# Kernel tuning notes

Hardware: AMD Instinct MI355X
Metric: run time of the kernel (lower is better)

The kernel has to match this reference:

```python
import jax, jax.numpy as jnp
import numpy as np

EPS = 1e-5

def setup_inputs() -> dict:
    key = jax.random.key(0)
    ks = jax.random.split(key, 8)
    B, T, D, S = 8, 4096, 1024, 64
    return {
        "x": jax.random.normal(ks[0], (B, T, D), dtype=jnp.float32),
        "time_decay": jax.random.normal(ks[1], (S,), dtype=jnp.float32) * 0.1 - 0.5,
        "time_first": jax.random.normal(ks[2], (S,), dtype=jnp.float32) * 0.1,
        "W_key": jax.random.normal(ks[3], (S, D), dtype=jnp.float32) * 0.02,
        "W_value": jax.random.normal(ks[4], (S, D), dtype=jnp.float32) * 0.02,
        "W_output": jax.random.normal(ks[5], (D, S), dtype=jnp.float32) * 0.02,
        "W_shift": jax.random.normal(ks[6], (D, D), dtype=jnp.float32) * 0.02,
        "shift_gate": jnp.ones((D,), dtype=jnp.float32),
        "ln_w": jnp.ones((D,), dtype=jnp.float32),
        "ln_b": jnp.zeros((D,), dtype=jnp.float32),
    }


def _forward(x, time_decay, time_first, W_key, W_value, W_output, W_shift, shift_gate, ln_w, ln_b):
    B, T, D = x.shape
    S = time_decay.shape[0]
    # --- token shift: rotate sequence by shift_len, project, gated blend ---
    shift_len = max(1, int(T * 0.5))
    x_cat = jnp.concatenate([x[:, shift_len:], x[:, :-shift_len]], axis=1)  # (B,T,D)
    gate = jax.nn.sigmoid(shift_gate)
    x_shift = jnp.einsum('btd,ed->bte', x_cat, W_shift) * gate + x * (1.0 - gate)
    # --- layernorm (torch: biased variance, eps=1e-5) ---
    mu = jnp.mean(x_shift, axis=-1, keepdims=True)
    var = jnp.mean(jnp.square(x_shift - mu), axis=-1, keepdims=True)
    xn = (x_shift - mu) * jax.lax.rsqrt(var + EPS) * ln_w + ln_b
    # --- key/value projections and per-step wkv (fully vectorized) ---
    k = jnp.einsum('btd,sd->bts', xn, W_key)    # (B,T,S)
    v = jnp.einsum('btd,sd->bts', xn, W_value)  # (B,T,S)
    wkv = jnp.exp(-jnp.exp(time_first) * jax.nn.sigmoid(k)) * v  # (B,T,S)
    # --- linear recurrence: state = state*w + wkv_t, scanned over T ---
    w = jnp.exp(time_decay)  # (S,)
    def step(state, wkv_t):
        state = state * w + wkv_t
        return state, state
    init = jnp.zeros((B, S), dtype=x.dtype)
    last_state, states = jax.lax.scan(step, init, jnp.swapaxes(wkv, 0, 1))  # states: (T,B,S)
    states = jnp.swapaxes(states, 0, 1)  # (B,T,S)
    # --- batched output projection (applied per-step in torch; same math) ---
    output = jnp.einsum('bts,ds->btd', states, W_output)  # (B,T,D)
    return output, last_state


def reference(x, time_decay, time_first, W_key, W_value, W_output, W_shift, shift_gate, ln_w, ln_b):
    out, last_state = _forward(x, time_decay, time_first, W_key, W_value, W_output, W_shift, shift_gate, ln_w, ln_b)
    return out, jax.lax.stop_gradient(last_state)
```

## Files before the change

### kernel.cpp

```cpp
#include <hip/hip_runtime.h>
#include <stdint.h>

#define B_ 8
#define T_ 4096
#define D_ 1024
#define S_ 64
#define N_ 32768
#define OUT_ELEMS 33554432
#define NCHK 128
#define CHKL 32

typedef __attribute__((ext_vector_type(8))) short bf16x8;
typedef __attribute__((ext_vector_type(8))) unsigned short u16x8;
typedef __attribute__((ext_vector_type(4))) float f32x4;

__device__ __forceinline__ uint16_t f2bf(float f) {
    union { float f; uint32_t u; } v; v.f = f;
    uint32_t r = v.u + 0x7FFFu + ((v.u >> 16) & 1u);
    return (uint16_t)(r >> 16);
}
__device__ __forceinline__ float bf2f(uint16_t h) {
    union { uint32_t u; float f; } v; v.u = ((uint32_t)h) << 16;
    return v.f;
}

#define GLOAD_LDS16(gp, lp)                                             \
    __builtin_amdgcn_global_load_lds(                                   \
        (const __attribute__((address_space(1))) void*)(gp),            \
        (__attribute__((address_space(3))) void*)(lp), 16, 0, 0)

__global__ void prep(const float* __restrict__ x,
                     const float* __restrict__ Wsf, const float* __restrict__ Wkf,
                     const float* __restrict__ Wvf, const float* __restrict__ Wof,
                     const float* __restrict__ sg, const float* __restrict__ tf,
                     const float* __restrict__ lnw, const float* __restrict__ lnb,
                     uint16_t* __restrict__ xb, uint16_t* __restrict__ Wsb,
                     uint16_t* __restrict__ Wkvb, uint16_t* __restrict__ Wob,
                     float* __restrict__ gbuf, float* __restrict__ efirst,
                     float* __restrict__ ucvec)
{
    __shared__ float red[4];
    const int blk = blockIdx.x, tid = threadIdx.x;
    if (blk < 2048) {
        for (int i = blk * 256 + tid; i < OUT_ELEMS / 4; i += 2048 * 256) {
            float4 v = ((const float4*)x)[i];
            ushort4 o;
            o.x = f2bf(v.x); o.y = f2bf(v.y); o.z = f2bf(v.z); o.w = f2bf(v.w);
            ((ushort4*)xb)[i] = o;
        }
        return;
    }
    if (blk < 3298) {
        int i = (blk - 2048) * 256 + tid;
        const float* src; uint16_t* dst; int j; bool fold = false;
        if (i < 262144) { src = Wsf; dst = Wsb; j = i; }
        else if (i < 278528) { src = Wkf; dst = Wkvb; j = i - 262144; fold = true; }
        else if (i < 294912) { src = Wvf; dst = Wkvb + 65536; j = i - 278528; fold = true; }
        else if (i < 311296) { src = Wof; dst = Wob; j = i - 294912; }
        else if (i < 311552) {
            j = i - 311296;
            float4 v = ((const float4*)sg)[j];
            float4 g;
            g.x = 1.f / (1.f + __expf(-v.x)); g.y = 1.f / (1.f + __expf(-v.y));
            g.z = 1.f / (1.f + __expf(-v.z)); g.w = 1.f / (1.f + __expf(-v.w));
            ((float4*)gbuf)[j] = g;
            return;
        } else if (i < 311568) {
            j = i - 311552;
            float4 v = ((const float4*)tf)[j];
            float4 e;
            e.x = __expf(v.x); e.y = __expf(v.y); e.z = __expf(v.z); e.w = __expf(v.w);
            ((float4*)efirst)[j] = e;
            return;
        } else return;
        float4 v = ((const float4*)src)[j];
        if (fold) {
            float4 l = ((const float4*)lnw)[j & 255];
            v.x *= l.x; v.y *= l.y; v.z *= l.z; v.w *= l.w;
        }
        ushort4 o;
        o.x = f2bf(v.x); o.y = f2bf(v.y); o.z = f2bf(v.z); o.w = f2bf(v.w);
        ((ushort4*)dst)[j] = o;
        return;
    }
    {
        int b2 = blk - 3298;
        int which = b2 >> 6, s = b2 & 63;
        const float* W = (which < 2) ? Wkf : Wvf;
        const float* L = (which & 1) ? lnb : lnw;
        float4 wv = ((const float4*)W)[s * 256 + tid];
        float4 lv = ((const float4*)L)[tid];
        float p = wv.x * lv.x + wv.y * lv.y + wv.z * lv.z + wv.w * lv.w;
#pragma unroll
        for (int off = 32; off; off >>= 1) p += __shfl_xor(p, off);
        if ((tid & 63) == 0) red[tid >> 6] = p;
        __syncthreads();
        if (tid == 0) ucvec[which * 64 + s] = red[0] + red[1] + red[2] + red[3];
    }
}

__global__ __launch_bounds__(512, 2) void k1_shift_gemm(
    const uint16_t* __restrict__ xb, const uint16_t* __restrict__ Wsb,
    const float* __restrict__ gbuf, uint16_t* __restrict__ xs)
{
    __shared__ char sh[131072];

    const int tid = threadIdx.x;
    const int w = tid >> 6, lane = tid & 63, quad = lane >> 4, l16 = lane & 15;
    const int wm = w >> 2, wn = w & 3;
    const int w8 = w * 8;

    const int lin = blockIdx.x;
    const int idx = lin >> 3;
    const int nt = idx & 3;
    const int mt = (lin & 7) * 16 + (idx >> 2);
    const int m0 = mt * 256, n0 = nt * 256;
    const int m0x = m0 ^ 2048;

    const int arow = w8 + (lane >> 3);
    const int scg  = ((lane & 7) ^ ((lane >> 3) & 7)) * 8;
    const uint16_t* aBase = xb  + (size_t)(m0x + arow) * D_ + scg;
    const uint16_t* bBase = Wsb + (size_t)(n0  + arow) * D_ + scg;

    const int swz0 = ((quad) ^ (l16 & 7)) * 8;
    const int swz1 = ((4 + quad) ^ (l16 & 7)) * 8;
    const int aRowBase = wm * 128 + l16;
    const int bRowBase = wn * 64 + l16;

    f32x4 acc[8][4];
#pragma unroll
    for (int i = 0; i < 8; ++i)
#pragma unroll
        for (int j = 0; j < 4; ++j) acc[i][j] = (f32x4){0.f, 0.f, 0.f, 0.f};

    {
        uint16_t (*A0)[64] = (uint16_t(*)[64])(sh);
        uint16_t (*B0)[64] = (uint16_t(*)[64])(sh + 32768);
#pragma unroll
        for (int c = 0; c < 4; ++c) {
            GLOAD_LDS16(aBase + (size_t)(c * 64) * D_, &A0[c * 64 + w8][0]);
            GLOAD_LDS16(bBase + (size_t)(c * 64) * D_, &B0[c * 64 + w8][0]);
        }
    }
    asm volatile("s_waitcnt vmcnt(0)" ::: "memory");
    __builtin_amdgcn_s_barrier();

#pragma unroll 1
    for (int t = 0; t < 16; ++t) {
        const int c = t & 1, o = c ^ 1;
        uint16_t (*Ac)[64] = (uint16_t(*)[64])(sh + c * 65536);
        uint16_t (*Bc)[64] = (uint16_t(*)[64])(sh + c * 65536 + 32768);
        uint16_t (*Ao)[64] = (uint16_t(*)[64])(sh + o * 65536);
        uint16_t (*Bo)[64] = (uint16_t(*)[64])(sh + o * 65536 + 32768);
        const int kb1 = (t + 1) * 64;

#pragma unroll
        for (int ks = 0; ks < 2; ++ks) {
            const int swz = ks ? swz1 : swz0;
            bf16x8 a[8], b[4];
#pragma unroll
            for (int mf = 0; mf < 8; ++mf)
                a[mf] = *(const bf16x8*)&Ac[aRowBase + mf * 16][swz];
#pragma unroll
            for (int nf = 0; nf < 4; ++nf)
                b[nf] = *(const bf16x8*)&Bc[bRowBase + nf * 16][swz];
            if (ks == 0 && t < 15) {
#pragma unroll
                for (int cc = 0; cc < 4; ++cc) {
                    GLOAD_LDS16(aBase + (size_t)(cc * 64) * D_ + kb1,
                                &Ao[cc * 64 + w8][0]);
                    GLOAD_LDS16(bBase + (size_t)(cc * 64) * D_ + kb1,
                                &Bo[cc * 64 + w8][0]);
                }
            }
            if (ks == 1 && t < 15) {
                asm volatile("s_waitcnt vmcnt(0)" ::: "memory");
            }
            __builtin_amdgcn_s_barrier();
            __builtin_amdgcn_s_setprio(1);
#pragma unroll
            for (int mf = 0; mf < 8; ++mf)
#pragma unroll
                for (int nf = 0; nf < 4; ++nf)
                    acc[mf][nf] = __builtin_amdgcn_mfma_f32_16x16x32_bf16(
                        a[mf], b[nf], acc[mf][nf], 0, 0, 0);
            __builtin_amdgcn_s_setprio(0);
        }
    }

    float (*epi)[260] = (float(*)[260])sh;
    const int row = tid >> 3;
    const int c0 = (tid & 7) * 32;
#pragma unroll
    for (int mb = 0; mb < 4; ++mb) {
        __syncthreads();
        if (wm == (mb >> 1)) {
#pragma unroll
            for (int mf = 0; mf < 4; ++mf)
#pragma unroll
                for (int nf = 0; nf < 4; ++nf)
#pragma unroll
                    for (int r = 0; r < 4; ++r)
                        epi[mf * 16 + quad * 4 + r][wn * 64 + nf * 16 + l16] =
                            acc[(mb & 1) * 4 + mf][nf][r];
        }
        __syncthreads();
        const int grow = m0 + mb * 64 + row;
        const uint16_t* xrow = xb + (size_t)grow * D_ + n0 + c0;
        uint16_t* orow = xs + (size_t)grow * D_ + n0 + c0;
#pragma unroll
        for (int c4 = 0; c4 < 8; ++c4) {
            float4 g4 = ((const float4*)(gbuf + n0 + c0))[c4];
            ushort4 xh = ((const ushort4*)xrow)[c4];
            const float* e = &epi[row][c0 + c4 * 4];
            ushort4 o;
            o.x = f2bf(e[0] * g4.x + bf2f(xh.x) * (1.f - g4.x));
            o.y = f2bf(e[1] * g4.y + bf2f(xh.y) * (1.f - g4.y));
            o.z = f2bf(e[2] * g4.z + bf2f(xh.z) * (1.f - g4.z));
            o.w = f2bf(e[3] * g4.w + bf2f(xh.w) * (1.f - g4.w));
            ((ushort4*)orow)[c4] = o;
        }
    }
}

__global__ __launch_bounds__(256) void k3_kv(
    const uint16_t* __restrict__ xsb, const uint16_t* __restrict__ Wkvb,
    const float* __restrict__ efirst, const float* __restrict__ ucvec,
    const float* __restrict__ time_decay,
    float* __restrict__ wkv, float* __restrict__ part)
{
    __shared__ char sh[52224];
    uint16_t (*As)[64] = (uint16_t(*)[64])sh;
    uint16_t (*Bs)[64] = (uint16_t(*)[64])(sh + 8192);
    float (*epi)[132] = (float(*)[132])sh;
    float* ssh = (float*)(sh + 33792);
    float* qsh = (float*)(sh + 34048);
    float (*wsh)[68] = (float(*)[68])(sh + 34816);

    const int tid = threadIdx.x;
    const int w = tid >> 6, lane = tid & 63, quad = lane >> 4, l16 = lane & 15;
    const int wm = w >> 1, wn = w & 1;
    const int m0 = blockIdx.x * 64;

    const int lrow = w * 8 + (lane >> 3);
    const int scg  = ((lane & 7) ^ ((lane >> 3) & 7)) * 8;
    const uint16_t* aG = xsb + (size_t)(m0 + lrow) * D_ + scg;
    const uint16_t* bG = Wkvb + (size_t)lrow * D_ + scg;

    f32x4 acc[2][4];
#pragma unroll
    for (int i = 0; i < 2; ++i)
#pragma unroll
        for (int j = 0; j < 4; ++j) acc[i][j] = (f32x4){0.f, 0.f, 0.f, 0.f};
    f32x4 accs[2], accq[2];
#pragma unroll
    for (int i = 0; i < 2; ++i) {
        accs[i] = (f32x4){0.f, 0.f, 0.f, 0.f};
        accq[i] = (f32x4){0.f, 0.f, 0.f, 0.f};
    }
    bf16x8 ones;
#pragma unroll
    for (int j = 0; j < 8; ++j) ones[j] = (short)0x3F80;

    for (int k0 = 0; k0 < D_; k0 += 64) {
        __syncthreads();
#pragma unroll
        for (int i = 0; i < 2; ++i)
            GLOAD_LDS16(aG + k0 + (size_t)(i * 32) * D_, &As[w * 8 + i * 32][0]);
#pragma unroll
        for (int i = 0; i < 4; ++i)
            GLOAD_LDS16(bG + k0 + (size_t)(i * 32) * D_, &Bs[w * 8 + i * 32][0]);
        __syncthreads();
#pragma unroll
        for (int ks = 0; ks < 2; ++ks) {
            bf16x8 a[2], b[4];
#pragma unroll
            for (int i = 0; i < 2; ++i)
                a[i] = *(const bf16x8*)&As[wm * 32 + i * 16 + l16]
                                         [(((ks * 4 + quad) ^ (l16 & 7)) * 8)];
#pragma unroll
            for (int j = 0; j < 4; ++j)
                b[j] = *(const bf16x8*)&Bs[wn * 64 + j * 16 + l16]
                                         [(((ks * 4 + quad) ^ (l16 & 7)) * 8)];
#pragma unroll
            for (int i = 0; i < 2; ++i)
#pragma unroll
                for (int j = 0; j < 4; ++j)
                    acc[i][j] = __builtin_amdgcn_mfma_f32_16x16x32_bf16(
                        a[i], b[j], acc[i][j], 0, 0, 0);
            if (wn == 0) {
#pragma unroll
                for (int i = 0; i < 2; ++i) {
                    accs[i] = __builtin_amdgcn_mfma_f32_16x16x32_bf16(
                        a[i], ones, accs[i], 0, 0, 0);
                    accq[i] = __builtin_amdgcn_mfma_f32_16x16x32_bf16(
                        a[i], a[i], accq[i], 0, 0, 0);
                }
            }
        }
    }

    if (wn == 0) {
#pragma unroll
        for (int i = 0; i < 2; ++i) {
            if (l16 == 0) {
#pragma unroll
                for (int r = 0; r < 4; ++r)
                    ssh[wm * 32 + i * 16 + quad * 4 + r] = accs[i][r];
            }
            if ((l16 >> 2) == quad)
                qsh[wm * 32 + i * 16 + l16] = accq[i][l16 & 3];
        }
    }

    __syncthreads();
#pragma unroll
    for (int i = 0; i < 2; ++i)
#pragma unroll
        for (int j = 0; j < 4; ++j)
#pragma unroll
            for (int r = 0; r < 4; ++r)
                epi[wm * 32 + i * 16 + quad * 4 + r][wn * 64 + j * 16 + l16] =
                    acc[i][j][r];
    __syncthreads();

    const int row = tid >> 2, s0 = (tid & 3) * 16;
    const float mu = ssh[row] * (1.f / (float)D_);
    const float var = qsh[row] * (1.f / (float)D_) - mu * mu;
    const float rstd = rsqrtf(var + 1e-5f);
    float* dst = wkv + (size_t)(m0 + row) * S_ + s0;
#pragma unroll
    for (int c4 = 0; c4 < 4; ++c4) {
        float4 kk = *(const float4*)&epi[row][s0 + c4 * 4];
        float4 vv = *(const float4*)&epi[row][64 + s0 + c4 * 4];
        float4 uk4 = *(const float4*)(ucvec + 0 * 64 + s0 + c4 * 4);
        float4 ck4 = *(const float4*)(ucvec + 1 * 64 + s0 + c4 * 4);
        float4 uv4 = *(const float4*)(ucvec + 2 * 64 + s0 + c4 * 4);
        float4 cv4 = *(const float4*)(ucvec + 3 * 64 + s0 + c4 * 4);
        float4 ef = ((const float4*)(efirst + s0))[c4];
        float kx = rstd * (kk.x - mu * uk4.x) + ck4.x;
        float ky = rstd * (kk.y - mu * uk4.y) + ck4.y;
        float kz = rstd * (kk.z - mu * uk4.z) + ck4.z;
        float kw = rstd * (kk.w - mu * uk4.w) + ck4.w;
        float vx = rstd * (vv.x - mu * uv4.x) + cv4.x;
        float vy = rstd * (vv.y - mu * uv4.y) + cv4.y;
        float vz = rstd * (vv.z - mu * uv4.z) + cv4.z;
        float vw = rstd * (vv.w - mu * uv4.w) + cv4.w;
        float4 o;
        o.x = __expf(-ef.x / (1.f + __expf(-kx))) * vx;
        o.y = __expf(-ef.y / (1.f + __expf(-ky))) * vy;
        o.z = __expf(-ef.z / (1.f + __expf(-kz))) * vz;
        o.w = __expf(-ef.w / (1.f + __expf(-kw))) * vw;
        *(float4*)(dst + c4 * 4) = o;
        *(float4*)&wsh[row][s0 + c4 * 4] = o;
    }

    __syncthreads();
    if (tid < 128) {
        const int ch = tid >> 6, s = tid & 63;
        const float w1 = expf(time_decay[s]);
        float st = 0.f;
#pragma unroll
        for (int t = 0; t < CHKL; ++t)
            st = st * w1 + wsh[ch * CHKL + t][s];
        const int b = m0 >> 12;
        const int gc = ((m0 & 4095) >> 5) + ch;
        part[((size_t)b * NCHK + gc) * S_ + s] = st;
    }
}

__global__ __launch_bounds__(256) void k5_out(
    const float* __restrict__ wkv, const float* __restrict__ part,
    const float* __restrict__ time_decay, const uint16_t* __restrict__ Wob,
    float* __restrict__ out, float* __restrict__ last_state)
{
    __shared__ char sh[34816];
    uint16_t (*stS)[64] = (uint16_t(*)[64])sh;
    float (*epi)[68] = (float(*)[68])sh;

    const int tid = threadIdx.x;
    const int w = tid >> 6, lane = tid & 63, quad = lane >> 4, l16 = lane & 15;
    const int wm = w >> 1, wn = w & 1;
    const int m0b = blockIdx.y * 128;
    const int n0b = blockIdx.x * 128;

    {
        const int b = m0b >> 12;
        const int c = ((m0b & 4095) >> 5) + w;
        const float td = time_decay[lane];
        const float w1 = expf(td);
        const float wL = expf(td * (float)CHKL);
        const float* pp = part + (size_t)b * NCHK * S_ + lane;
        float cin = 0.f;
        for (int j = 0; j < c; ++j) cin = cin * wL + pp[(size_t)j * S_];
        const float* src = wkv + (size_t)(m0b + w * CHKL) * S_ + lane;
        float st = cin;
#pragma unroll
        for (int t = 0; t < CHKL; ++t) {
            st = st * w1 + src[(size_t)t * S_];
            const int row = w * CHKL + t;
            stS[row][(((lane >> 3) ^ (row & 7)) << 3) | (lane & 7)] = f2bf(st);
        }
        if (n0b == 0 && c == NCHK - 1)
            last_state[b * S_ + lane] = st;
    }
    __syncthreads();

    f32x4 acc[4][4];
#pragma unroll
    for (int i = 0; i < 4; ++i)
#pragma unroll
        for (int j = 0; j < 4; ++j) acc[i][j] = (f32x4){0.f, 0.f, 0.f, 0.f};

#pragma unroll
    for (int k = 0; k < S_; k += 32) {
        bf16x8 a[4], b[4];
#pragma unroll
        for (int i = 0; i < 4; ++i) {
            const int row = wm * 64 + i * 16 + l16;
            a[i] = *(const bf16x8*)&stS[row]
                       [((((k >> 3) + quad) ^ (l16 & 7)) * 8)];
        }
#pragma unroll
        for (int i = 0; i < 4; ++i)
            b[i] = *(const bf16x8*)(Wob + (size_t)(n0b + wn * 64 + i * 16 + l16) * S_ + k + quad * 8);
#pragma unroll
        for (int i = 0; i < 4; ++i)
#pragma unroll
            for (int j = 0; j < 4; ++j)
                acc[i][j] = __builtin_amdgcn_mfma_f32_16x16x32_bf16(
                    a[i], b[j], acc[i][j], 0, 0, 0);
    }

    const int row = tid >> 1;
    const int c0 = (tid & 1) * 32;
#pragma unroll
    for (int h = 0; h < 2; ++h) {
        __syncthreads();
        if (wn == h) {
#pragma unroll
            for (int i = 0; i < 4; ++i)
#pragma unroll
                for (int j = 0; j < 4; ++j)
#pragma unroll
                    for (int r = 0; r < 4; ++r)
                        epi[wm * 64 + i * 16 + quad * 4 + r][j * 16 + l16] =
                            acc[i][j][r];
        }
        __syncthreads();
        float* dst = out + (size_t)(m0b + row) * D_ + n0b + h * 64 + c0;
#pragma unroll
        for (int c4 = 0; c4 < 8; ++c4)
            ((float4*)dst)[c4] = *(const float4*)&epi[row][c0 + c4 * 4];
    }
}

extern "C" void kernel_launch(void* const* d_in, const int* in_sizes, int n_in,
                              void* d_out, int out_size, void* d_ws, size_t ws_size,
                              hipStream_t stream) {
    const float* x          = (const float*)d_in[0];
    const float* time_decay = (const float*)d_in[1];
    const float* time_first = (const float*)d_in[2];
    const float* W_key      = (const float*)d_in[3];
    const float* W_value    = (const float*)d_in[4];
    const float* W_output   = (const float*)d_in[5];
    const float* W_shift    = (const float*)d_in[6];
    const float* shift_gate = (const float*)d_in[7];
    const float* ln_w       = (const float*)d_in[8];
    const float* ln_b       = (const float*)d_in[9];
    float* out = (float*)d_out;

    char* ws = (char*)d_ws;
    uint16_t* xb      = (uint16_t*)(ws + 0);
    uint16_t* xs      = (uint16_t*)(ws + 67108864);
    float*    wkv     = (float*)   (ws + 134217728);
    uint16_t* Wsb     = (uint16_t*)(ws + 146800640);
    uint16_t* Wkvb    = (uint16_t*)(ws + 148897792);
    uint16_t* Wob     = (uint16_t*)(ws + 149159936);
    float*    part    = (float*)   (ws + 149291008);
    float*    gbuf    = (float*)   (ws + 149815296);
    float*    efirst  = (float*)   (ws + 149819392);
    float*    ucvec   = (float*)   (ws + 149819648);

    prep<<<3554, 256, 0, stream>>>(x, W_shift, W_key, W_value, W_output,
                                   shift_gate, time_first, ln_w, ln_b,
                                   xb, Wsb, Wkvb, Wob, gbuf, efirst, ucvec);
    k1_shift_gemm<<<512, 512, 0, stream>>>(xb, Wsb, gbuf, xs);
    k3_kv<<<512, 256, 0, stream>>>(xs, Wkvb, efirst, ucvec, time_decay,
                                   wkv, part);
    k5_out<<<dim3(8, 256), 256, 0, stream>>>(wkv, part, time_decay, Wob,
                                             out, out + OUT_ELEMS);
}
```

Measured before the change: 434.7 us.

## Double-buffer k3 GEMM loads and reuse chunk-state prefix across k5 column tiles

The k3_kv K-loop now double-buffers its LDS tiles. The next tile's global-to-LDS loads are issued while the current tile's MFMAs run, with raised wave priority around the MFMA block and wsh aliased onto the freed epilogue region. k5_out drops from 8 to 2 column blocks per row tile, and each block loops over 4 N-tiles, so the serial chunk-prefix scan and per-chunk state build are done 4x less often. The trade-off is less grid parallelism in k5 (512 blocks) and a different LDS layout, since the epilogue buffer is moved off the state tile.

```diff
diff --git a/kernel.cpp b/kernel.cpp
--- a/kernel.cpp
+++ b/kernel.cpp
@@ -229,23 +229,26 @@
     const float* __restrict__ time_decay,
     float* __restrict__ wkv, float* __restrict__ part)
 {
-    __shared__ char sh[52224];
-    uint16_t (*As)[64] = (uint16_t(*)[64])sh;
-    uint16_t (*Bs)[64] = (uint16_t(*)[64])(sh + 8192);
+    __shared__ char sh[49664];
     float (*epi)[132] = (float(*)[132])sh;
-    float* ssh = (float*)(sh + 33792);
-    float* qsh = (float*)(sh + 34048);
-    float (*wsh)[68] = (float(*)[68])(sh + 34816);
+    float* ssh = (float*)(sh + 49152);
+    float* qsh = (float*)(sh + 49408);
 
     const int tid = threadIdx.x;
     const int w = tid >> 6, lane = tid & 63, quad = lane >> 4, l16 = lane & 15;
     const int wm = w >> 1, wn = w & 1;
+    const int w8 = w * 8;
     const int m0 = blockIdx.x * 64;
 
-    const int lrow = w * 8 + (lane >> 3);
+    const int arow = w8 + (lane >> 3);
     const int scg  = ((lane & 7) ^ ((lane >> 3) & 7)) * 8;
-    const uint16_t* aG = xsb + (size_t)(m0 + lrow) * D_ + scg;
-    const uint16_t* bG = Wkvb + (size_t)lrow * D_ + scg;
+    const uint16_t* aBase = xsb + (size_t)(m0 + arow) * D_ + scg;
+    const uint16_t* bBase = Wkvb + (size_t)arow * D_ + scg;
+
+    const int swz0 = ((quad) ^ (l16 & 7)) * 8;
+    const int swz1 = ((4 + quad) ^ (l16 & 7)) * 8;
+    const int aRowBase = wm * 32 + l16;
+    const int bRowBase = wn * 64 + l16;
 
     f32x4 acc[2][4];
 #pragma unroll
@@ -262,41 +265,69 @@
 #pragma unroll
     for (int j = 0; j < 8; ++j) ones[j] = (short)0x3F80;
 
-    for (int k0 = 0; k0 < D_; k0 += 64) {
-        __syncthreads();
-#pragma unroll
-        for (int i = 0; i < 2; ++i)
-            GLOAD_LDS16(aG + k0 + (size_t)(i * 32) * D_, &As[w * 8 + i * 32][0]);
-#pragma unroll
-        for (int i = 0; i < 4; ++i)
-            GLOAD_LDS16(bG + k0 + (size_t)(i * 32) * D_, &Bs[w * 8 + i * 32][0]);
-        __syncthreads();
+    {
+        uint16_t (*A0)[64] = (uint16_t(*)[64])(sh);
+        uint16_t (*B0)[64] = (uint16_t(*)[64])(sh + 8192);
+#pragma unroll
+        for (int c = 0; c < 2; ++c)
+            GLOAD_LDS16(aBase + (size_t)(c * 32) * D_, &A0[c * 32 + w8][0]);
+#pragma unroll
+        for (int c = 0; c < 4; ++c)
+            GLOAD_LDS16(bBase + (size_t)(c * 32) * D_, &B0[c * 32 + w8][0]);
+    }
+    asm volatile("s_waitcnt vmcnt(0)" ::: "memory");
+    __builtin_amdgcn_s_barrier();
+
+#pragma unroll 1
+    for (int t = 0; t < 16; ++t) {
+        const int c = t & 1, o = c ^ 1;
+        uint16_t (*Ac)[64] = (uint16_t(*)[64])(sh + c * 24576);
+        uint16_t (*Bc)[64] = (uint16_t(*)[64])(sh + c * 24576 + 8192);
+        uint16_t (*Ao)[64] = (uint16_t(*)[64])(sh + o * 24576);
+        uint16_t (*Bo)[64] = (uint16_t(*)[64])(sh + o * 24576 + 8192);
+        const int kb1 = (t + 1) * 64;
+
 #pragma unroll
         for (int ks = 0; ks < 2; ++ks) {
+            const int swz = ks ? swz1 : swz0;
             bf16x8 a[2], b[4];
 #pragma unroll
-            for (int i = 0; i < 2; ++i)
-                a[i] = *(const bf16x8*)&As[wm * 32 + i * 16 + l16]
-                                         [(((ks * 4 + quad) ^ (l16 & 7)) * 8)];
-#pragma unroll
-            for (int j = 0; j < 4; ++j)
-                b[j] = *(const bf16x8*)&Bs[wn * 64 + j * 16 + l16]
-                                         [(((ks * 4 + quad) ^ (l16 & 7)) * 8)];
-#pragma unroll
-            for (int i = 0; i < 2; ++i)
-#pragma unroll
-                for (int j = 0; j < 4; ++j)
-                    acc[i][j] = __builtin_amdgcn_mfma_f32_16x16x32_bf16(
-                        a[i], b[j], acc[i][j], 0, 0, 0);
+            for (int mf = 0; mf < 2; ++mf)
+                a[mf] = *(const bf16x8*)&Ac[aRowBase + mf * 16][swz];
+#pragma unroll
+            for (int nf = 0; nf < 4; ++nf)
+                b[nf] = *(const bf16x8*)&Bc[bRowBase + nf * 16][swz];
+            if (ks == 0 && t < 15) {
+#pragma unroll
+                for (int cc = 0; cc < 2; ++cc)
+                    GLOAD_LDS16(aBase + (size_t)(cc * 32) * D_ + kb1,
+                                &Ao[cc * 32 + w8][0]);
+#pragma unroll
+                for (int cc = 0; cc < 4; ++cc)
+                    GLOAD_LDS16(bBase + (size_t)(cc * 32) * D_ + kb1,
+                                &Bo[cc * 32 + w8][0]);
+            }
+            if (ks == 1 && t < 15) {
+                asm volatile("s_waitcnt vmcnt(0)" ::: "memory");
+            }
+            __builtin_amdgcn_s_barrier();
+            __builtin_amdgcn_s_setprio(1);
+#pragma unroll
+            for (int mf = 0; mf < 2; ++mf)
+#pragma unroll
+                for (int nf = 0; nf < 4; ++nf)
+                    acc[mf][nf] = __builtin_amdgcn_mfma_f32_16x16x32_bf16(
+                        a[mf], b[nf], acc[mf][nf], 0, 0, 0);
             if (wn == 0) {
 #pragma unroll
-                for (int i = 0; i < 2; ++i) {
-                    accs[i] = __builtin_amdgcn_mfma_f32_16x16x32_bf16(
-                        a[i], ones, accs[i], 0, 0, 0);
-                    accq[i] = __builtin_amdgcn_mfma_f32_16x16x32_bf16(
-                        a[i], a[i], accq[i], 0, 0, 0);
+                for (int mf = 0; mf < 2; ++mf) {
+                    accs[mf] = __builtin_amdgcn_mfma_f32_16x16x32_bf16(
+                        a[mf], ones, accs[mf], 0, 0, 0);
+                    accq[mf] = __builtin_amdgcn_mfma_f32_16x16x32_bf16(
+                        a[mf], a[mf], accq[mf], 0, 0, 0);
                 }
             }
+            __builtin_amdgcn_s_setprio(0);
         }
     }
 
@@ -352,7 +383,7 @@
         o.z = __expf(-ef.z / (1.f + __expf(-kz))) * vz;
         o.w = __expf(-ef.w / (1.f + __expf(-kw))) * vw;
         *(float4*)(dst + c4 * 4) = o;
-        *(float4*)&wsh[row][s0 + c4 * 4] = o;
+        *(float4*)&epi[row][s0 + c4 * 4] = o;
     }
 
     __syncthreads();
@@ -362,7 +393,7 @@
         float st = 0.f;
 #pragma unroll
         for (int t = 0; t < CHKL; ++t)
-            st = st * w1 + wsh[ch * CHKL + t][s];
+            st = st * w1 + epi[ch * CHKL + t][s];
         const int b = m0 >> 12;
         const int gc = ((m0 & 4095) >> 5) + ch;
         part[((size_t)b * NCHK + gc) * S_ + s] = st;
@@ -374,15 +405,15 @@
     const float* __restrict__ time_decay, const uint16_t* __restrict__ Wob,
     float* __restrict__ out, float* __restrict__ last_state)
 {
-    __shared__ char sh[34816];
+    __shared__ char sh[51200];
     uint16_t (*stS)[64] = (uint16_t(*)[64])sh;
-    float (*epi)[68] = (float(*)[68])sh;
+    float (*epi)[68] = (float(*)[68])(sh + 16384);
 
     const int tid = threadIdx.x;
     const int w = tid >> 6, lane = tid & 63, quad = lane >> 4, l16 = lane & 15;
     const int wm = w >> 1, wn = w & 1;
     const int m0b = blockIdx.y * 128;
-    const int n0b = blockIdx.x * 128;
+    const int h = blockIdx.x;
 
     {
         const int b = m0b >> 12;
@@ -392,6 +423,7 @@
         const float wL = expf(td * (float)CHKL);
         const float* pp = part + (size_t)b * NCHK * S_ + lane;
         float cin = 0.f;
+#pragma unroll 4
         for (int j = 0; j < c; ++j) cin = cin * wL + pp[(size_t)j * S_];
         const float* src = wkv + (size_t)(m0b + w * CHKL) * S_ + lane;
         float st = cin;
@@ -401,57 +433,61 @@
             const int row = w * CHKL + t;
             stS[row][(((lane >> 3) ^ (row & 7)) << 3) | (lane & 7)] = f2bf(st);
         }
-        if (n0b == 0 && c == NCHK - 1)
+        if (h == 0 && c == NCHK - 1)
             last_state[b * S_ + lane] = st;
     }
     __syncthreads();
 
-    f32x4 acc[4][4];
-#pragma unroll
-    for (int i = 0; i < 4; ++i)
-#pragma unroll
-        for (int j = 0; j < 4; ++j) acc[i][j] = (f32x4){0.f, 0.f, 0.f, 0.f};
-
-#pragma unroll
-    for (int k = 0; k < S_; k += 32) {
-        bf16x8 a[4], b[4];
-#pragma unroll
-        for (int i = 0; i < 4; ++i) {
-            const int row = wm * 64 + i * 16 + l16;
-            a[i] = *(const bf16x8*)&stS[row]
-                       [((((k >> 3) + quad) ^ (l16 & 7)) * 8)];
-        }
+#pragma unroll 1
+    for (int nt = 0; nt < 4; ++nt) {
+        const int n0b = h * 512 + nt * 128;
+        f32x4 acc[4][4];
 #pragma unroll
         for (int i = 0; i < 4; ++i)
-            b[i] = *(const bf16x8*)(Wob + (size_t)(n0b + wn * 64 + i * 16 + l16) * S_ + k + quad * 8);
-#pragma unroll
-        for (int i = 0; i < 4; ++i)
-#pragma unroll
-            for (int j = 0; j < 4; ++j)
-                acc[i][j] = __builtin_amdgcn_mfma_f32_16x16x32_bf16(
-                    a[i], b[j], acc[i][j], 0, 0, 0);
-    }
-
-    const int row = tid >> 1;
-    const int c0 = (tid & 1) * 32;
-#pragma unroll
-    for (int h = 0; h < 2; ++h) {
-        __syncthreads();
-        if (wn == h) {
+#pragma unroll
+            for (int j = 0; j < 4; ++j) acc[i][j] = (f32x4){0.f, 0.f, 0.f, 0.f};
+
+#pragma unroll
+        for (int k = 0; k < S_; k += 32) {
+            bf16x8 a[4], b[4];
+#pragma unroll
+            for (int i = 0; i < 4; ++i) {
+                const int row = wm * 64 + i * 16 + l16;
+                a[i] = *(const bf16x8*)&stS[row]
+                           [((((k >> 3) + quad) ^ (l16 & 7)) * 8)];
+            }
 #pragma unroll
             for (int i = 0; i < 4; ++i)
+                b[i] = *(const bf16x8*)(Wob + (size_t)(n0b + wn * 64 + i * 16 + l16) * S_ + k + quad * 8);
+#pragma unroll
+            for (int i = 0; i < 4; ++i)
 #pragma unroll
                 for (int j = 0; j < 4; ++j)
-#pragma unroll
-                    for (int r = 0; r < 4; ++r)
-                        epi[wm * 64 + i * 16 + quad * 4 + r][j * 16 + l16] =
-                            acc[i][j][r];
-        }
-        __syncthreads();
-        float* dst = out + (size_t)(m0b + row) * D_ + n0b + h * 64 + c0;
-#pragma unroll
-        for (int c4 = 0; c4 < 8; ++c4)
-            ((float4*)dst)[c4] = *(const float4*)&epi[row][c0 + c4 * 4];
+                    acc[i][j] = __builtin_amdgcn_mfma_f32_16x16x32_bf16(
+                        a[i], b[j], acc[i][j], 0, 0, 0);
+        }
+
+        const int row = tid >> 1;
+        const int c0 = (tid & 1) * 32;
+#pragma unroll
+        for (int hh = 0; hh < 2; ++hh) {
+            __syncthreads();
+            if (wn == hh) {
+#pragma unroll
+                for (int i = 0; i < 4; ++i)
+#pragma unroll
+                    for (int j = 0; j < 4; ++j)
+#pragma unroll
+                        for (int r = 0; r < 4; ++r)
+                            epi[wm * 64 + i * 16 + quad * 4 + r][j * 16 + l16] =
+                                acc[i][j][r];
+            }
+            __syncthreads();
+            float* dst = out + (size_t)(m0b + row) * D_ + n0b + hh * 64 + c0;
+#pragma unroll
+            for (int c4 = 0; c4 < 8; ++c4)
+                ((float4*)dst)[c4] = *(const float4*)&epi[row][c0 + c4 * 4];
+        }
     }
 }
 
@@ -488,6 +524,6 @@
     k1_shift_gemm<<<512, 512, 0, stream>>>(xb, Wsb, gbuf, xs);
     k3_kv<<<512, 256, 0, stream>>>(xs, Wkvb, efirst, ucvec, time_decay,
                                    wkv, part);
-    k5_out<<<dim3(8, 256), 256, 0, stream>>>(wkv, part, time_decay, Wob,
+    k5_out<<<dim3(2, 256), 256, 0, stream>>>(wkv, part, time_decay, Wob,
                                              out, out + OUT_ELEMS);
 }
```

New measurement: 410.8 us. 5.5% less time.
